# Kernel tuning notes

Measured on AMD Instinct MI355X. Metric: run time of the kernel, lower is better.

## Reference

```python
import jax, jax.numpy as jnp
import numpy as np

N, C, T, H, W = 8, 3, 32, 256, 256
K = 5  # kernel size, pad = K // 2 ('same' output size)


def _dw_conv_last(x2, w):
    """Depthwise 1D cross-correlation along last axis.
    x2: [B, C, L], w: [C, K] -> [B, C, L] (zero 'same' padding).
    Matches torch.nn.Conv1d(groups=C, bias=False, padding=K//2)."""
    pad = w.shape[1] // 2
    return jax.lax.conv_general_dilated(
        x2, w[:, None, :],  # kernel [O=C, I=1, K]
        window_strides=(1,), padding=[(pad, pad)],
        dimension_numbers=('NCH', 'OIH', 'NCH'),
        feature_group_count=w.shape[0])


def _conv_along(x, w, axis):
    """Depthwise conv of [N,C,T,H,W] along `axis` (2, 3 or 4)."""
    y = jnp.moveaxis(x, axis, -1)   # [N, C, a, b, L]
    y = jnp.moveaxis(y, 1, -2)      # [N, a, b, C, L]
    sh = y.shape
    y = _dw_conv_last(y.reshape(-1, sh[3], sh[4]), w).reshape(sh)
    y = jnp.moveaxis(y, -2, 1)      # [N, C, a, b, L]
    return jnp.moveaxis(y, -1, axis)


def setup_inputs() -> dict:
    key = jax.random.key(0)
    kx, k1, k2, k3 = jax.random.split(key, 4)
    return {
        'x': jax.random.normal(kx, (N, C, T, H, W), dtype=jnp.float32),
        'w1': jax.random.normal(k1, (C, K), dtype=jnp.float32),  # along W
        'w2': jax.random.normal(k2, (C, K), dtype=jnp.float32),  # along H
        'w3': jax.random.normal(k3, (C, K), dtype=jnp.float32),  # along T
    }


def reference(x, w1, w2, w3):
    # Axis-separable depthwise 3D conv: W, then H, then T (as in SeparableConv3D).
    x = _conv_along(x, w1, 4)
    x = _conv_along(x, w2, 3)
    x = _conv_along(x, w3, 2)
    return x  # [N, C, T, H, W]
```

## Files before the change

kernel.cpp:

```cpp
#include <hip/hip_runtime.h>


#define N_  8
#define C_  3
#define T_  32
#define H_  256
#define W_  256
#define K_  5
#define HW_ (H_ * W_)

#define TH 16
#define TW 64
#define SX_PAD_FLOATS 1536

__global__ __launch_bounds__(256)
void sep3d_fused2(const float* __restrict__ x,
                  const float* __restrict__ w1,
                  const float* __restrict__ w2,
                  const float* __restrict__ w3,
                  float* __restrict__ out)
{
    __shared__ float4 sx4[SX_PAD_FLOATS / 4];
    __shared__ float4 sy4[20 * (TW / 4)];
    float* sx = (float*)sx4;

    const int tid = threadIdx.x;
    const int nc  = blockIdx.z;
    const int c   = nc % C_;
    const int h0  = blockIdx.y * TH;
    const int w0  = blockIdx.x * TW;

    const float* xnc = x   + (size_t)nc * (T_ * HW_);
    float*       onc = out + (size_t)nc * (T_ * HW_);

    float k1[K_], k2[K_], k3[K_];
#pragma unroll
    for (int k = 0; k < K_; ++k) {
        k1[k] = w1[c * K_ + k];
        k2[k] = w2[c * K_ + k];
        k3[k] = w3[c * K_ + k];
    }

    int  s1_off[6];
    bool s1_ok[6];
#pragma unroll
    for (int j = 0; j < 6; ++j) {
        int i   = tid + j * 256;
        int row = i / 68;
        int col = i - row * 68;
        int gh  = h0 + row - 2;
        int gw  = w0 + col - 2;
        s1_ok[j]  = (i < 1360) && ((unsigned)gh < H_) && ((unsigned)gw < W_);
        s1_off[j] = gh * W_ + gw;
    }

    const int row3 = tid >> 4;
    const int seg3 = tid & 15;
    float* gst = onc + (h0 + row3) * W_ + (w0 + 4 * seg3);

    float4 a0 = {0,0,0,0}, a1 = a0, a2 = a0, a3 = a0;

    for (int t = 0; t < T_; ++t) {
        const float* xt = xnc + (size_t)t * HW_;

#pragma unroll
        for (int j = 0; j < 6; ++j) {
            float v = 0.0f;
            if (s1_ok[j]) v = xt[s1_off[j]];
            sx[tid + j * 256] = v;
        }
        __syncthreads();

#pragma unroll
        for (int rep = 0; rep < 2; ++rep) {
            int task = tid + rep * 256;
            if (task < 320) {
                int seg = task & 15, row = task >> 4;
                const float4* p = (const float4*)&sx[row * 68 + 4 * seg];
                float4 aa = p[0], bb = p[1];
                float xv0 = aa.x, xv1 = aa.y, xv2 = aa.z, xv3 = aa.w;
                float xv4 = bb.x, xv5 = bb.y, xv6 = bb.z, xv7 = bb.w;
                float4 y;
                y.x = xv0*k1[0] + xv1*k1[1] + xv2*k1[2] + xv3*k1[3] + xv4*k1[4];
                y.y = xv1*k1[0] + xv2*k1[1] + xv3*k1[2] + xv4*k1[3] + xv5*k1[4];
                y.z = xv2*k1[0] + xv3*k1[1] + xv4*k1[2] + xv5*k1[3] + xv6*k1[4];
                y.w = xv3*k1[0] + xv4*k1[1] + xv5*k1[2] + xv6*k1[3] + xv7*k1[4];
                sy4[row * 16 + seg] = y;
            }
        }
        __syncthreads();

        float4 z = {0,0,0,0};
#pragma unroll
        for (int k = 0; k < K_; ++k) {
            float4 r = sy4[(row3 + k) * 16 + seg3];
            z.x += r.x * k2[k];
            z.y += r.y * k2[k];
            z.z += r.z * k2[k];
            z.w += r.w * k2[k];
        }

        float4 done;
        done.x = a0.x + z.x * k3[4];
        done.y = a0.y + z.y * k3[4];
        done.z = a0.z + z.z * k3[4];
        done.w = a0.w + z.w * k3[4];
        if (t >= 2) *(float4*)(gst + (size_t)(t - 2) * HW_) = done;
        a0.x = a1.x + z.x * k3[3];  a0.y = a1.y + z.y * k3[3];
        a0.z = a1.z + z.z * k3[3];  a0.w = a1.w + z.w * k3[3];
        a1.x = a2.x + z.x * k3[2];  a1.y = a2.y + z.y * k3[2];
        a1.z = a2.z + z.z * k3[2];  a1.w = a2.w + z.w * k3[2];
        a2.x = a3.x + z.x * k3[1];  a2.y = a3.y + z.y * k3[1];
        a2.z = a3.z + z.z * k3[1];  a2.w = a3.w + z.w * k3[1];
        a3.x = z.x * k3[0];  a3.y = z.y * k3[0];
        a3.z = z.z * k3[0];  a3.w = z.w * k3[0];
    }

    *(float4*)(gst + (size_t)30 * HW_) = a0;
    *(float4*)(gst + (size_t)31 * HW_) = a1;
}

extern "C" void kernel_launch(void* const* d_in, const int* in_sizes, int n_in,
                              void* d_out, int out_size, void* d_ws, size_t ws_size,
                              hipStream_t stream)
{
    const float* x  = (const float*)d_in[0];
    const float* w1 = (const float*)d_in[1];
    const float* w2 = (const float*)d_in[2];
    const float* w3 = (const float*)d_in[3];
    float* out = (float*)d_out;

    dim3 grid(W_ / TW, H_ / TH, N_ * C_);
    sep3d_fused2<<<grid, 256, 0, stream>>>(x, w1, w2, w3, out);
}
```

Measured before the change: 432.6 us.

## Double-buffer shared tiles, prefetch next frame into registers, use nontemporal stores

Shared input and intermediate tiles become double-buffered. The next time-slice is loaded into registers two steps ahead, so global loads overlap with compute and one __syncthreads per step is removed. The intermediate row stride is padded to 17 to change the LDS bank pattern, and output stores become nontemporal to avoid polluting the cache. This costs extra LDS and registers, which may lower occupancy.

```diff
diff --git a/kernel.cpp b/kernel.cpp
--- a/kernel.cpp
+++ b/kernel.cpp
@@ -12,17 +12,20 @@
 #define TH 16
 #define TW 64
 #define SX_PAD_FLOATS 1536
+#define SY_ROWS   20
+#define SY_STRIDE 17
+
+typedef float nfloat4 __attribute__((ext_vector_type(4)));
 
 __global__ __launch_bounds__(256)
-void sep3d_fused2(const float* __restrict__ x,
+void sep3d_fused3(const float* __restrict__ x,
                   const float* __restrict__ w1,
                   const float* __restrict__ w2,
                   const float* __restrict__ w3,
                   float* __restrict__ out)
 {
-    __shared__ float4 sx4[SX_PAD_FLOATS / 4];
-    __shared__ float4 sy4[20 * (TW / 4)];
-    float* sx = (float*)sx4;
+    __shared__ float4 sx4[2][SX_PAD_FLOATS / 4];
+    __shared__ float4 sy4[2][SY_ROWS * SY_STRIDE];
 
     const int tid = threadIdx.x;
     const int nc  = blockIdx.z;
@@ -60,24 +63,31 @@
 
     float4 a0 = {0,0,0,0}, a1 = a0, a2 = a0, a3 = a0;
 
+    float p[6];
+    {
+#pragma unroll
+        for (int j = 0; j < 6; ++j) p[j] = s1_ok[j] ? xnc[s1_off[j]] : 0.0f;
+        float* sx0 = (float*)sx4[0];
+#pragma unroll
+        for (int j = 0; j < 6; ++j) sx0[tid + j * 256] = p[j];
+        const float* xt1 = xnc + (size_t)HW_;
+#pragma unroll
+        for (int j = 0; j < 6; ++j) p[j] = s1_ok[j] ? xt1[s1_off[j]] : 0.0f;
+    }
+    __syncthreads();
+
     for (int t = 0; t < T_; ++t) {
-        const float* xt = xnc + (size_t)t * HW_;
-
-#pragma unroll
-        for (int j = 0; j < 6; ++j) {
-            float v = 0.0f;
-            if (s1_ok[j]) v = xt[s1_off[j]];
-            sx[tid + j * 256] = v;
-        }
-        __syncthreads();
+        const int cur = t & 1;
+        float* sxc = (float*)sx4[cur];
+        float* sxn = (float*)sx4[cur ^ 1];
 
 #pragma unroll
         for (int rep = 0; rep < 2; ++rep) {
             int task = tid + rep * 256;
             if (task < 320) {
                 int seg = task & 15, row = task >> 4;
-                const float4* p = (const float4*)&sx[row * 68 + 4 * seg];
-                float4 aa = p[0], bb = p[1];
+                const float4* pp = (const float4*)&sxc[row * 68 + 4 * seg];
+                float4 aa = pp[0], bb = pp[1];
                 float xv0 = aa.x, xv1 = aa.y, xv2 = aa.z, xv3 = aa.w;
                 float xv4 = bb.x, xv5 = bb.y, xv6 = bb.z, xv7 = bb.w;
                 float4 y;
@@ -85,27 +95,41 @@
                 y.y = xv1*k1[0] + xv2*k1[1] + xv3*k1[2] + xv4*k1[3] + xv5*k1[4];
                 y.z = xv2*k1[0] + xv3*k1[1] + xv4*k1[2] + xv5*k1[3] + xv6*k1[4];
                 y.w = xv3*k1[0] + xv4*k1[1] + xv5*k1[2] + xv6*k1[3] + xv7*k1[4];
-                sy4[row * 16 + seg] = y;
+                sy4[cur][row * SY_STRIDE + seg] = y;
             }
         }
+
+#pragma unroll
+        for (int j = 0; j < 6; ++j) sxn[tid + j * 256] = p[j];
+
         __syncthreads();
+
+        if (t + 2 < T_) {
+            const float* xt = xnc + (size_t)(t + 2) * HW_;
+#pragma unroll
+            for (int j = 0; j < 6; ++j) p[j] = s1_ok[j] ? xt[s1_off[j]] : 0.0f;
+        } else {
+#pragma unroll
+            for (int j = 0; j < 6; ++j) p[j] = 0.0f;
+        }
 
         float4 z = {0,0,0,0};
 #pragma unroll
         for (int k = 0; k < K_; ++k) {
-            float4 r = sy4[(row3 + k) * 16 + seg3];
+            float4 r = sy4[cur][(row3 + k) * SY_STRIDE + seg3];
             z.x += r.x * k2[k];
             z.y += r.y * k2[k];
             z.z += r.z * k2[k];
             z.w += r.w * k2[k];
         }
 
-        float4 done;
+        nfloat4 done;
         done.x = a0.x + z.x * k3[4];
         done.y = a0.y + z.y * k3[4];
         done.z = a0.z + z.z * k3[4];
         done.w = a0.w + z.w * k3[4];
-        if (t >= 2) *(float4*)(gst + (size_t)(t - 2) * HW_) = done;
+        if (t >= 2)
+            __builtin_nontemporal_store(done, (nfloat4*)(gst + (size_t)(t - 2) * HW_));
         a0.x = a1.x + z.x * k3[3];  a0.y = a1.y + z.y * k3[3];
         a0.z = a1.z + z.z * k3[3];  a0.w = a1.w + z.w * k3[3];
         a1.x = a2.x + z.x * k3[2];  a1.y = a2.y + z.y * k3[2];
@@ -116,8 +140,11 @@
         a3.z = z.z * k3[0];  a3.w = z.w * k3[0];
     }
 
-    *(float4*)(gst + (size_t)30 * HW_) = a0;
-    *(float4*)(gst + (size_t)31 * HW_) = a1;
+    nfloat4 e0, e1;
+    e0.x = a0.x; e0.y = a0.y; e0.z = a0.z; e0.w = a0.w;
+    e1.x = a1.x; e1.y = a1.y; e1.z = a1.z; e1.w = a1.w;
+    __builtin_nontemporal_store(e0, (nfloat4*)(gst + (size_t)30 * HW_));
+    __builtin_nontemporal_store(e1, (nfloat4*)(gst + (size_t)31 * HW_));
 }
 
 extern "C" void kernel_launch(void* const* d_in, const int* in_sizes, int n_in,
@@ -131,5 +158,5 @@
     float* out = (float*)d_out;
 
     dim3 grid(W_ / TW, H_ / TH, N_ * C_);
-    sep3d_fused2<<<grid, 256, 0, stream>>>(x, w1, w2, w3, out);
+    sep3d_fused3<<<grid, 256, 0, stream>>>(x, w1, w2, w3, out);
 }
```

After: 363.8 us. 15.9% less time.

## Use per-wave double-buffered tiles with register prefetch and no block barriers

Applied to the files above, without the earlier changes.

Each wave now independently processes a 4-row strip, keeping its own double-buffered shared tile filled from float2 register prefetches two time steps ahead. This removes block-wide __syncthreads and overlaps global loads with compute. The W-direction conv is recomputed per H tap instead of staged, and output stores become nontemporal. It trades more halo reads and arithmetic, and reliance on wave-synchronous LDS behavior, for latency hiding.

```diff
diff --git a/kernel.cpp b/kernel.cpp
--- a/kernel.cpp
+++ b/kernel.cpp
@@ -11,23 +11,27 @@
 
 #define TH 16
 #define TW 64
-#define SX_PAD_FLOATS 1536
+#define XSTR 68
+#define XF2  272
+#define XPADF 640
+
+typedef float nfloat4 __attribute__((ext_vector_type(4)));
 
 __global__ __launch_bounds__(256)
-void sep3d_fused2(const float* __restrict__ x,
-                  const float* __restrict__ w1,
-                  const float* __restrict__ w2,
-                  const float* __restrict__ w3,
-                  float* __restrict__ out)
+void sep3d_wave(const float* __restrict__ x,
+                const float* __restrict__ w1,
+                const float* __restrict__ w2,
+                const float* __restrict__ w3,
+                float* __restrict__ out)
 {
-    __shared__ float4 sx4[SX_PAD_FLOATS / 4];
-    __shared__ float4 sy4[20 * (TW / 4)];
-    float* sx = (float*)sx4;
+    __shared__ float sxAll[4][2][XPADF];
 
     const int tid = threadIdx.x;
+    const int wv  = tid >> 6;
+    const int ln  = tid & 63;
     const int nc  = blockIdx.z;
     const int c   = nc % C_;
-    const int h0  = blockIdx.y * TH;
+    const int h0  = blockIdx.y * TH + wv * 4;
     const int w0  = blockIdx.x * TW;
 
     const float* xnc = x   + (size_t)nc * (T_ * HW_);
@@ -41,83 +45,95 @@
         k3[k] = w3[c * K_ + k];
     }
 
-    int  s1_off[6];
-    bool s1_ok[6];
+    int  goff[5];
+    bool gok[5];
+    int  loff[5];
 #pragma unroll
-    for (int j = 0; j < 6; ++j) {
-        int i   = tid + j * 256;
-        int row = i / 68;
-        int col = i - row * 68;
-        int gh  = h0 + row - 2;
-        int gw  = w0 + col - 2;
-        s1_ok[j]  = (i < 1360) && ((unsigned)gh < H_) && ((unsigned)gw < W_);
-        s1_off[j] = gh * W_ + gw;
+    for (int j = 0; j < 5; ++j) {
+        int i   = ln + 64 * j;
+        int row = i / 34;
+        int c2  = i - row * 34;
+        int gh  = h0 - 2 + row;
+        int gw  = w0 - 2 + 2 * c2;
+        gok[j]  = (i < XF2) && ((unsigned)gh < H_) && (gw >= 0) && (gw + 1 < W_);
+        goff[j] = gok[j] ? (gh * W_ + gw) : 0;
+        loff[j] = 2 * i;
     }
 
-    const int row3 = tid >> 4;
-    const int seg3 = tid & 15;
-    float* gst = onc + (h0 + row3) * W_ + (w0 + 4 * seg3);
+    const int r0 = ln >> 4;
+    const int s3 = ln & 15;
+    float* gst = onc + (size_t)(h0 + r0) * W_ + (w0 + 4 * s3);
 
-    float4 a0 = {0,0,0,0}, a1 = a0, a2 = a0, a3 = a0;
+    nfloat4 a0 = {0,0,0,0}, a1 = a0, a2 = a0, a3 = a0;
 
-    for (int t = 0; t < T_; ++t) {
-        const float* xt = xnc + (size_t)t * HW_;
+    float2 pA[5], pB[5];
 
-#pragma unroll
-        for (int j = 0; j < 6; ++j) {
-            float v = 0.0f;
-            if (s1_ok[j]) v = xt[s1_off[j]];
-            sx[tid + j * 256] = v;
-        }
-        __syncthreads();
+#define LOADP(P, tt) do {                                                   \
+    const int tc_ = ((tt) < T_) ? (tt) : 0;                                 \
+    const bool tok_ = (tt) < T_;                                            \
+    const float* xt_ = xnc + (size_t)tc_ * HW_;                             \
+    _Pragma("unroll") for (int j = 0; j < 5; ++j) {                         \
+        float2 v_ = *(const float2*)(xt_ + goff[j]);                        \
+        bool ok_ = tok_ && gok[j];                                          \
+        (P)[j].x = ok_ ? v_.x : 0.0f;                                       \
+        (P)[j].y = ok_ ? v_.y : 0.0f;                                       \
+    } } while (0)
 
-#pragma unroll
-        for (int rep = 0; rep < 2; ++rep) {
-            int task = tid + rep * 256;
-            if (task < 320) {
-                int seg = task & 15, row = task >> 4;
-                const float4* p = (const float4*)&sx[row * 68 + 4 * seg];
-                float4 aa = p[0], bb = p[1];
-                float xv0 = aa.x, xv1 = aa.y, xv2 = aa.z, xv3 = aa.w;
-                float xv4 = bb.x, xv5 = bb.y, xv6 = bb.z, xv7 = bb.w;
-                float4 y;
-                y.x = xv0*k1[0] + xv1*k1[1] + xv2*k1[2] + xv3*k1[3] + xv4*k1[4];
-                y.y = xv1*k1[0] + xv2*k1[1] + xv3*k1[2] + xv4*k1[3] + xv5*k1[4];
-                y.z = xv2*k1[0] + xv3*k1[1] + xv4*k1[2] + xv5*k1[3] + xv6*k1[4];
-                y.w = xv3*k1[0] + xv4*k1[1] + xv5*k1[2] + xv6*k1[3] + xv7*k1[4];
-                sy4[row * 16 + seg] = y;
-            }
-        }
-        __syncthreads();
+#define WRITEP(P, B) do {                                                   \
+    float* sw_ = &sxAll[wv][(B)][0];                                        \
+    _Pragma("unroll") for (int j = 0; j < 5; ++j)                           \
+        *(float2*)(sw_ + loff[j]) = (P)[j];                                 \
+    } while (0)
 
-        float4 z = {0,0,0,0};
-#pragma unroll
-        for (int k = 0; k < K_; ++k) {
-            float4 r = sy4[(row3 + k) * 16 + seg3];
-            z.x += r.x * k2[k];
-            z.y += r.y * k2[k];
-            z.z += r.z * k2[k];
-            z.w += r.w * k2[k];
-        }
+#define COMPUTE(B, tt) do {                                                 \
+    const float* sr_ = &sxAll[wv][(B)][0];                                  \
+    nfloat4 z = {0,0,0,0};                                                  \
+    _Pragma("unroll") for (int k = 0; k < K_; ++k) {                        \
+        const float4* pp = (const float4*)(sr_ + (r0 + k) * XSTR + 4 * s3); \
+        float4 aa = pp[0], bb = pp[1];                                      \
+        float y0 = aa.x*k1[0]+aa.y*k1[1]+aa.z*k1[2]+aa.w*k1[3]+bb.x*k1[4];  \
+        float y1 = aa.y*k1[0]+aa.z*k1[1]+aa.w*k1[2]+bb.x*k1[3]+bb.y*k1[4];  \
+        float y2 = aa.z*k1[0]+aa.w*k1[1]+bb.x*k1[2]+bb.y*k1[3]+bb.z*k1[4];  \
+        float y3 = aa.w*k1[0]+bb.x*k1[1]+bb.y*k1[2]+bb.z*k1[3]+bb.w*k1[4];  \
+        z.x += y0 * k2[k]; z.y += y1 * k2[k];                               \
+        z.z += y2 * k2[k]; z.w += y3 * k2[k];                               \
+    }                                                                       \
+    nfloat4 dn;                                                             \
+    dn.x = a0.x + z.x * k3[4]; dn.y = a0.y + z.y * k3[4];                   \
+    dn.z = a0.z + z.z * k3[4]; dn.w = a0.w + z.w * k3[4];                   \
+    if ((tt) >= 2)                                                          \
+        __builtin_nontemporal_store(dn,                                     \
+            (nfloat4*)(gst + (size_t)((tt) - 2) * HW_));                    \
+    a0.x = a1.x + z.x * k3[3]; a0.y = a1.y + z.y * k3[3];                   \
+    a0.z = a1.z + z.z * k3[3]; a0.w = a1.w + z.w * k3[3];                   \
+    a1.x = a2.x + z.x * k3[2]; a1.y = a2.y + z.y * k3[2];                   \
+    a1.z = a2.z + z.z * k3[2]; a1.w = a2.w + z.w * k3[2];                   \
+    a2.x = a3.x + z.x * k3[1]; a2.y = a3.y + z.y * k3[1];                   \
+    a2.z = a3.z + z.z * k3[1]; a2.w = a3.w + z.w * k3[1];                   \
+    a3.x = z.x * k3[0]; a3.y = z.y * k3[0];                                 \
+    a3.z = z.z * k3[0]; a3.w = z.w * k3[0];                                 \
+    } while (0)
 
-        float4 done;
-        done.x = a0.x + z.x * k3[4];
-        done.y = a0.y + z.y * k3[4];
-        done.z = a0.z + z.z * k3[4];
-        done.w = a0.w + z.w * k3[4];
-        if (t >= 2) *(float4*)(gst + (size_t)(t - 2) * HW_) = done;
-        a0.x = a1.x + z.x * k3[3];  a0.y = a1.y + z.y * k3[3];
-        a0.z = a1.z + z.z * k3[3];  a0.w = a1.w + z.w * k3[3];
-        a1.x = a2.x + z.x * k3[2];  a1.y = a2.y + z.y * k3[2];
-        a1.z = a2.z + z.z * k3[2];  a1.w = a2.w + z.w * k3[2];
-        a2.x = a3.x + z.x * k3[1];  a2.y = a3.y + z.y * k3[1];
-        a2.z = a3.z + z.z * k3[1];  a2.w = a3.w + z.w * k3[1];
-        a3.x = z.x * k3[0];  a3.y = z.y * k3[0];
-        a3.z = z.z * k3[0];  a3.w = z.w * k3[0];
+    LOADP(pA, 0);
+    WRITEP(pA, 0);
+    LOADP(pA, 1);
+    LOADP(pB, 2);
+
+    for (int t = 0; t < T_; t += 2) {
+        COMPUTE(0, t);
+        WRITEP(pA, 1);
+        LOADP(pA, t + 3);
+        COMPUTE(1, t + 1);
+        WRITEP(pB, 0);
+        LOADP(pB, t + 4);
     }
 
-    *(float4*)(gst + (size_t)30 * HW_) = a0;
-    *(float4*)(gst + (size_t)31 * HW_) = a1;
+    __builtin_nontemporal_store(a0, (nfloat4*)(gst + (size_t)30 * HW_));
+    __builtin_nontemporal_store(a1, (nfloat4*)(gst + (size_t)31 * HW_));
+
+#undef LOADP
+#undef WRITEP
+#undef COMPUTE
 }
 
 extern "C" void kernel_launch(void* const* d_in, const int* in_sizes, int n_in,
@@ -131,5 +147,5 @@
     float* out = (float*)d_out;
 
     dim3 grid(W_ / TW, H_ / TH, N_ * C_);
-    sep3d_fused2<<<grid, 256, 0, stream>>>(x, w1, w2, w3, out);
+    sep3d_wave<<<grid, 256, 0, stream>>>(x, w1, w2, w3, out);
 }
```

After: 375.9 us. 13.1% less time.
